# Performance work log

Hardware: AMD Instinct MI355X
Metric: run time of the kernel (lower is better)

## Reference

```python
import jax, jax.numpy as jnp
import numpy as np

_SAMPLING_EPS = 1e-5


def _apply_top_p_top_k(logits, p, k):
    # Descending sort over vocab, as in the torch.jit.script kernel.
    sort_idx = jnp.argsort(logits, axis=-1)[:, ::-1]            # [B, V]
    logits_sort = jnp.take_along_axis(logits, sort_idx, axis=-1)
    probs_sort = jax.nn.softmax(logits_sort, axis=-1)
    probs_sum = jnp.cumsum(probs_sort, axis=-1)
    ar = jnp.arange(logits.shape[-1], dtype=jnp.int32)
    mask = (probs_sum - probs_sort > p[:, None]) | (ar[None, :] >= k[:, None])
    logits_sort = jnp.where(mask, -jnp.inf, logits_sort)
    # Scatter back to original token order via inverse permutation.
    inv_idx = jnp.argsort(sort_idx, axis=-1)
    return jnp.take_along_axis(logits_sort, inv_idx, axis=-1)


def _apply_min_p(logits, min_p):
    probs = jax.nn.softmax(logits, axis=-1)
    top_probs = probs.max(axis=-1, keepdims=True)
    remove = probs < min_p[:, None] * top_probs
    return jnp.where(remove, -jnp.inf, logits)


def setup_inputs() -> dict:
    key = jax.random.key(0)
    ks = jax.random.split(key, 6)
    B, V = 128, 128000
    logits = jax.random.normal(ks[0], (B, V), dtype=jnp.float32) * 2.0
    temperatures = jax.random.uniform(ks[1], (B,), minval=0.5, maxval=1.5, dtype=jnp.float32)
    top_ps = jax.random.uniform(ks[2], (B,), minval=0.5, maxval=1.0, dtype=jnp.float32)
    top_ks = jax.random.randint(ks[3], (B,), 1, 1024, dtype=jnp.int32)
    min_ps = jax.random.uniform(ks[4], (B,), minval=0.0, maxval=0.1, dtype=jnp.float32)
    # q = Exponential(1); torch does probs * q^{-1} then argmax -> argmax(probs / q)
    exp_noise = jax.random.exponential(ks[5], (B, V), dtype=jnp.float32)
    return {"logits": logits, "temperatures": temperatures, "top_ps": top_ps,
            "top_ks": top_ks, "min_ps": min_ps, "exp_noise": exp_noise}


def reference(logits, temperatures, top_ps, top_ks, min_ps, exp_noise):
    # Greedy rows (temp < eps) are scaled by 1.0 in the original sampler.
    temps = jnp.where(temperatures < _SAMPLING_EPS, 1.0, temperatures)
    x = logits / temps[:, None]
    k = jnp.maximum(top_ks, 1)  # top_k == -1 maps to vocab_size upstream
    x = _apply_top_p_top_k(x, top_ps, k)
    x = _apply_min_p(x, min_ps)
    logprobs = jax.nn.log_softmax(x, axis=-1)
    probs = jnp.exp(logprobs)
    # exponential-trick multinomial sampling: argmax(probs * Exp(1)^{-1})
    sampled_tokens = jnp.argmax(probs / exp_noise, axis=-1)
    return sampled_tokens, probs, logprobs
```

## Files before the change

kernel.cpp:

```cpp
#include <hip/hip_runtime.h>
#include <cmath>

#define BROWS 128
#define VCOLS 128000
#define XHI 24.0f
#define BIN_INV 1.5238095f
#define CAP2 2048
#define ACAP 2048
#define LCAP 2048

__device__ __forceinline__ unsigned enc32(float x){
  unsigned b = __float_as_uint(x);
  return (b & 0x80000000u) ? ~b : (b | 0x80000000u);
}
__device__ __forceinline__ float dec32(unsigned e){
  unsigned b = (e & 0x80000000u) ? (e & 0x7FFFFFFFu) : ~e;
  return __uint_as_float(b);
}
__device__ __forceinline__ unsigned long long csel(unsigned long long a, unsigned long long b, bool keepmax){
  unsigned long long mx = a > b ? a : b;
  unsigned long long mn = a > b ? b : a;
  return keepmax ? mx : mn;
}
__device__ __forceinline__ void wagg_append(bool pred, unsigned long long key,
                                            int* cnt, unsigned long long* buf, int cap, int lane){
  unsigned long long mk = __ballot(pred);
  if (mk){
    int leader = __ffsll((long long)mk) - 1;
    int base;
    if (lane == leader) base = atomicAdd(cnt, __popcll(mk));
    base = __shfl(base, leader);
    if (pred){
      int pos = base + __popcll(mk & ((1ull << lane) - 1ull));
      if (pos < cap) buf[pos] = key;
    }
  }
}

__device__ __forceinline__ int binOf(float x){
  return (int)((XHI - x) * BIN_INV);
}

__global__ __launch_bounds__(256)
void k12_stats_collect(const float* __restrict__ logits, const float* __restrict__ temps,
                       const int* __restrict__ topks,
                       float* __restrict__ maxpart, float* __restrict__ spart,
                       unsigned* __restrict__ histpart,
                       unsigned long long* __restrict__ candbuf, int* __restrict__ ncc, int segc)
{
  const int bid = blockIdx.x;
  const int r = bid >> 3, c = bid & 7;
  const int tid = threadIdx.x, lane = tid & 63, col = tid & 31;
  __shared__ unsigned sh[2048];
  __shared__ float redm[4], reds[4];
  __shared__ unsigned long long lcand[LCAP];
  __shared__ int lcnt, sJsel;
  for (int i = tid; i < 2048; i += 256) sh[i] = 0u;
  if (tid == 0) lcnt = 0;
  __syncthreads();
  float t = temps[r]; if (t < 1e-5f) t = 1.0f;
  const float it = 1.0f / t;
  int kk = topks[r]; if (kk < 1) kk = 1;
  const float4* src = (const float4*)(logits + (size_t)r*VCOLS + c*16000);
  float mx = -INFINITY, s = 0.f;
  for (int f = tid; f < 4000; f += 256){
    float4 v = src[f];
    #pragma unroll
    for (int e = 0; e < 4; e++){
      float x = ((const float*)&v)[e] * it;
      mx = fmaxf(mx, x);
      s += __expf(x - XHI);
      int b = binOf(x);
      if (b < 64){ if (b < 0) b = 0; atomicAdd(&sh[(b<<5)+col], 1u); }
    }
  }
  #pragma unroll
  for (int o = 32; o > 0; o >>= 1){
    mx = fmaxf(mx, __shfl_down(mx, o));
    s += __shfl_down(s, o);
  }
  if (lane == 0){ redm[tid>>6] = mx; reds[tid>>6] = s; }
  __syncthreads();
  if (tid == 0){
    maxpart[bid] = fmaxf(fmaxf(redm[0], redm[1]), fmaxf(redm[2], redm[3]));
    spart[bid]   = reds[0] + reds[1] + reds[2] + reds[3];
  }
  if (tid < 64){
    unsigned cnt = 0;
    #pragma unroll
    for (int q = 0; q < 32; q++) cnt += sh[(tid<<5) + ((q + tid) & 31)];
    histpart[bid*64 + tid] = cnt;
    unsigned inc = cnt;
    #pragma unroll
    for (int o = 1; o < 64; o <<= 1){ unsigned v2 = __shfl_up(inc, o); if (lane >= o) inc += v2; }
    unsigned long long ball = __ballot(inc >= (unsigned)kk);
    if (tid == 0) sJsel = ball ? (__ffsll((long long)ball) - 1) : 63;
  }
  __syncthreads();
  const float thrJ = (float)(sJsel + 1);
  const int jbase = c*16000;
  {
    int f = tid;
    float4 v = src[f];
    while (true){
      int fn = f + 256;
      bool more = fn < 4000;
      float4 vn;
      if (more) vn = src[fn];
      #pragma unroll
      for (int e = 0; e < 4; e++){
        float x = ((const float*)&v)[e] * it;
        float vv = (XHI - x) * BIN_INV;
        bool pred = vv < thrJ;
        unsigned long long key = ((unsigned long long)enc32(x) << 32) | (unsigned)(jbase + 4*f + e);
        wagg_append(pred, key, &lcnt, lcand, LCAP, lane);
      }
      if (!more) break;
      v = vn; f = fn;
    }
  }
  __syncthreads();
  int n = lcnt; if (n > LCAP) n = LCAP; if (n > segc) n = segc;
  if (tid == 0) ncc[bid] = n;
  unsigned long long* dst = candbuf + (size_t)bid*segc;
  for (int i = tid; i < n; i += 256) dst[i] = lcand[i];
}

__global__ __launch_bounds__(1024)
void k3_select(const float* __restrict__ temps,
               const float* __restrict__ topps, const int* __restrict__ topks,
               const float* __restrict__ minps,
               const float* __restrict__ maxpart, const float* __restrict__ spart,
               const unsigned* __restrict__ histpart,
               const unsigned long long* __restrict__ candbuf, const int* __restrict__ ncc, int segc,
               const float* __restrict__ noise, float* __restrict__ out)
{
  const int r = blockIdx.x;
  const int tid = threadIdx.x;
  const int lane = tid & 63;
  __shared__ unsigned long long buf2[CAP2];
  __shared__ unsigned long long actA[ACAP];
  __shared__ unsigned long long actB[ACAP];
  __shared__ float sM, sS, sP, sMinp, sSp, swsum[16];
  __shared__ float sLogZ, sZsum;
  __shared__ int sK, sJsel, sN2, sNact, sNact2, sFbSel, sTot, sM1, sM2;
  __shared__ unsigned sFh[16];
  __shared__ unsigned long long spk[16];

  if (tid == 0){
    float M = -INFINITY; float ssum = 0.f;
    #pragma unroll
    for (int c2 = 0; c2 < 8; c2++) M = fmaxf(M, maxpart[8*r + c2]);
    #pragma unroll
    for (int c2 = 0; c2 < 8; c2++) ssum += spart[8*r + c2];
    sM = M;
    sS = expf(XHI - M) * ssum;
    int kk = topks[r]; if (kk < 1) kk = 1; sK = kk;
    sP = topps[r]; sMinp = minps[r];
    sN2 = 0; sNact = 0;
  }
  {
    int kk0 = topks[r]; if (kk0 < 1) kk0 = 1;
    if (tid < 64){
      unsigned cnt = 0;
      #pragma unroll
      for (int c2 = 0; c2 < 8; c2++) cnt += histpart[(8*r + c2)*64 + tid];
      unsigned inc = cnt;
      #pragma unroll
      for (int o = 1; o < 64; o <<= 1){ unsigned v = __shfl_up(inc, o); if (lane >= o) inc += v; }
      unsigned long long ball = __ballot(inc >= (unsigned)kk0);
      if (tid == 0) sJsel = ball ? (__ffsll((long long)ball) - 1) : 63;
    }
  }
  __syncthreads();
  const float M = sM, S = sS;
  const int kk = sK, jsel = sJsel;
  const float thrJ = (float)(jsel + 1);
  const float vLoJ = (float)jsel;
  for (int c2 = 0; c2 < 8; c2++){
    int nc = ncc[8*r + c2]; if (nc > segc) nc = segc;
    const unsigned long long* seg = candbuf + (size_t)(8*r + c2)*segc;
    int ncr = (nc + 1023) & ~1023;
    for (int i = tid; i < ncr; i += 1024){
      bool in = i < nc;
      unsigned long long key = in ? seg[i] : 0ull;
      float vv = 0.f;
      if (in){
        float x = dec32((unsigned)(key >> 32));
        vv = (XHI - x) * BIN_INV;
      }
      bool toBuf = in && (vv < vLoJ);
      bool toAct = in && !(vv < vLoJ) && (vv < thrJ);
      wagg_append(toBuf, key, &sN2, buf2, CAP2, lane);
      wagg_append(toAct, key, &sNact, actA, ACAP, lane);
    }
  }
  __syncthreads();
  int n2c  = sN2   < CAP2 ? sN2   : CAP2;
  int nact = sNact < ACAP ? sNact : ACAP;
  unsigned long long* cur = actA;
  unsigned long long* nxt = actB;
  float vLo = vLoJ, W = 1.0f;
  bool doneRoute = false;
  for (int lev = 0; lev < 4 && !doneRoute; ++lev){
    if (n2c + nact <= 1024) break;
    if (tid < 16) sFh[tid] = 0u;
    __syncthreads();
    const float inv = 16.0f / W;
    const float w16 = W * 0.0625f;
    const int nr = (nact + 1023) & ~1023;
    for (int i = tid; i < nr; i += 1024){
      if (i < nact){
        float x = dec32((unsigned)(cur[i] >> 32));
        float vv = (XHI - x) * BIN_INV;
        int fb = (int)((vv - vLo) * inv);
        fb = fb < 0 ? 0 : (fb > 15 ? 15 : fb);
        atomicAdd(&sFh[fb], 1u);
      }
    }
    __syncthreads();
    if (tid < 64){
      unsigned incv = (lane < 16) ? sFh[lane] : 0u;
      #pragma unroll
      for (int o = 1; o < 16; o <<= 1){ unsigned u = __shfl_up(incv, o); if (lane >= o) incv += u; }
      unsigned long long ball = __ballot((lane < 16) && (n2c + (int)incv >= kk));
      int fbS = ball ? (__ffsll((long long)ball) - 1) : 15;
      if (lane == fbS){ sFbSel = fbS; sTot = n2c + (int)incv; }
    }
    __syncthreads();
    const int fbSel = sFbSel;
    const int tot = sTot;
    const bool finalR = (tot <= 1024) || (lev == 3);
    if (tid == 0) sNact2 = 0;
    __syncthreads();
    for (int i = tid; i < nr; i += 1024){
      bool in = i < nact;
      unsigned long long key = in ? cur[i] : 0ull;
      int fb = 16;
      if (in){
        float x = dec32((unsigned)(key >> 32));
        float vv = (XHI - x) * BIN_INV;
        fb = (int)((vv - vLo) * inv);
        fb = fb < 0 ? 0 : (fb > 15 ? 15 : fb);
      }
      bool toBuf = in && ((fb < fbSel) || (finalR && fb == fbSel));
      bool toAct = in && !finalR && (fb == fbSel);
      wagg_append(toBuf, key, &sN2, buf2, CAP2, lane);
      wagg_append(toAct, key, &sNact2, nxt, ACAP, lane);
    }
    __syncthreads();
    n2c = sN2 < CAP2 ? sN2 : CAP2;
    if (finalR){ nact = 0; doneRoute = true; }
    else {
      nact = sNact2 < ACAP ? sNact2 : ACAP;
      unsigned long long* t2 = cur; cur = nxt; nxt = t2;
      vLo = vLo + (float)fbSel * w16;
      W = w16;
    }
  }
  if (nact > 0){
    for (int i = tid; i < nact; i += 1024){
      int pos = n2c + i; if (pos < CAP2) buf2[pos] = cur[i];
    }
    n2c = (n2c + nact < CAP2) ? (n2c + nact) : CAP2;
  }
  __syncthreads();
  const int n2 = n2c;
  const int sortN = (n2 <= 1024) ? 1024 : 2048;
  for (int i = n2 + tid; i < sortN; i += 1024) buf2[i] = 0ull;
  __syncthreads();
  if (sortN == 1024){
    unsigned long long a = buf2[tid];
    for (int ks = 2; ks <= 1024; ks <<= 1){
      for (int j = ks >> 1; j > 0; j >>= 1){
        if (j >= 64){
          __syncthreads();
          buf2[tid] = a;
          __syncthreads();
          unsigned long long b = buf2[tid ^ j];
          bool km = ((tid & ks) == 0) == ((tid & j) == 0);
          a = csel(a, b, km);
        } else {
          unsigned long long b = __shfl_xor(a, j);
          bool km = ((tid & ks) == 0) == ((lane & j) == 0);
          a = csel(a, b, km);
        }
      }
    }
    __syncthreads();
    buf2[tid] = a;
    __syncthreads();
  } else {
    unsigned long long a0 = buf2[tid], a1 = buf2[tid + 1024];
    const int i1 = tid + 1024;
    for (int ks = 2; ks <= 2048; ks <<= 1){
      for (int j = ks >> 1; j > 0; j >>= 1){
        if (j == 1024){
          unsigned long long mx = a0 > a1 ? a0 : a1;
          unsigned long long mn = a0 > a1 ? a1 : a0;
          a0 = mx; a1 = mn;
        } else if (j >= 64){
          __syncthreads();
          buf2[tid] = a0; buf2[i1] = a1;
          __syncthreads();
          unsigned long long b0 = buf2[tid ^ j];
          unsigned long long b1 = buf2[i1 ^ j];
          bool km0 = ((tid & ks) == 0) == ((tid & j) == 0);
          bool km1 = ((i1  & ks) == 0) == ((i1  & j) == 0);
          a0 = csel(a0, b0, km0);
          a1 = csel(a1, b1, km1);
        } else {
          unsigned long long b0 = __shfl_xor(a0, j);
          unsigned long long b1 = __shfl_xor(a1, j);
          bool lw = ((lane & j) == 0);
          bool km0 = (((tid & ks) == 0) == lw);
          bool km1 = (((i1  & ks) == 0) == lw);
          a0 = csel(a0, b0, km0);
          a1 = csel(a1, b1, km1);
        }
      }
    }
    __syncthreads();
    buf2[tid] = a0; buf2[i1] = a1;
    __syncthreads();
  }
  const int kk2 = kk < n2 ? kk : n2;
  if (tid == 0) sM1 = kk2;
  unsigned long long mykey = 0ull;
  float xv = 0.f, qq = 0.f;
  if (tid < kk2){
    mykey = buf2[tid];
    xv = dec32((unsigned)(mykey >> 32));
    qq = expf(xv - M);
  }
  float inc = qq;
  #pragma unroll
  for (int o = 1; o < 64; o <<= 1){ float v = __shfl_up(inc, o); if (lane >= o) inc += v; }
  if (lane == 63) swsum[tid >> 6] = inc;
  __syncthreads();
  if (tid < 16){
    float v = swsum[tid];
    #pragma unroll
    for (int o = 1; o < 16; o <<= 1){ float u = __shfl_up(v, o); if (lane >= o) v += u; }
    swsum[tid] = v;
  }
  __syncthreads();
  float epre = __shfl_up(inc, 1); if (lane == 0) epre = 0.f;
  const int wvi = tid >> 6;
  const float excl = (wvi ? swsum[wvi - 1] : 0.f) + epre;
  const float pS = sP * S;
  if (tid < kk2 && !(excl <= pS)) atomicMin(&sM1, tid);
  __syncthreads();
  const int m = sM1 > 0 ? sM1 : 1;
  if (tid == m) sSp = excl;
  if (tid == 0) sM2 = m;
  __syncthreads();
  const float Sp = sSp;
  {
    float rhs = sMinp * (1.0f / Sp);
    if (tid < m && (qq / Sp < rhs)) atomicMin(&sM2, tid);
  }
  __syncthreads();
  const int m2 = sM2 > 0 ? sM2 : 1;
  if (tid == m2) sZsum = excl;
  __syncthreads();
  if (tid == 0) sLogZ = logf(sZsum);
  __syncthreads();
  {
    const float logZ = sLogZ;
    unsigned long long pk = 0ull;
    if (tid < m2){
      unsigned idx = (unsigned)(mykey & 0xFFFFFFFFull);
      float lp = (xv - M) - logZ;
      float pr = expf(lp);
      out[128 + (size_t)r*VCOLS + idx] = pr;
      out[128 + (size_t)BROWS*VCOLS + (size_t)r*VCOLS + idx] = lp;
      float nz = noise[(size_t)r*VCOLS + idx];
      float ratio = pr / nz;
      pk = ((unsigned long long)__float_as_uint(ratio) << 32) | (unsigned)(~idx);
    }
    #pragma unroll
    for (int o = 32; o > 0; o >>= 1){
      unsigned long long other = __shfl_down(pk, o);
      if (other > pk) pk = other;
    }
    if (lane == 0) spk[tid >> 6] = pk;
    __syncthreads();
    if (tid == 0){
      unsigned long long b0 = spk[0];
      #pragma unroll
      for (int w = 1; w < 16; w++) if (spk[w] > b0) b0 = spk[w];
      out[r] = (float)(~(unsigned)(b0 & 0xFFFFFFFFull));
    }
  }
}

extern "C" void kernel_launch(void* const* d_in, const int* in_sizes, int n_in,
                              void* d_out, int out_size, void* d_ws, size_t ws_size,
                              hipStream_t stream) {
  const float* logits = (const float*)d_in[0];
  const float* temps  = (const float*)d_in[1];
  const float* topps  = (const float*)d_in[2];
  const int*   topks  = (const int*)d_in[3];
  const float* minps  = (const float*)d_in[4];
  const float* noise  = (const float*)d_in[5];
  float* out = (float*)d_out;
  char* ws = (char*)d_ws;
  float* maxpart = (float*)(ws);
  float* spart   = (float*)(ws + 4096);
  int* ncc       = (int*)(ws + 8192);
  unsigned* histpart = (unsigned*)(ws + 12288);
  unsigned long long* candbuf = (unsigned long long*)(ws + 274432);
  int segc = 2048;
  if (ws_size < (size_t)274432 + 1024ull*2048ull*8ull) segc = 1536;
  if (ws_size < (size_t)274432 + 1024ull*1536ull*8ull) segc = 512;

  k12_stats_collect<<<1024, 256, 0, stream>>>(logits, temps, topks,
                                              maxpart, spart, histpart, candbuf, ncc, segc);
  k3_select<<<128, 1024, 0, stream>>>(temps, topps, topks, minps,
                                      maxpart, spart, histpart, candbuf, ncc, segc,
                                      noise, out);
}
```

Measured before the change: 258.0 us.

## Prefetch logits loads, flatten candidate gather, merge top-p and min-p cutoffs

The first pass now double-buffers float4 loads two iterations ahead so global loads overlap the histogram and exp work. In the select kernel, segment offsets are prefix-summed once so all candidates are gathered in one flat loop instead of eight padded per-segment loops. The histogram scan moves to a second wavefront. The min-p test is rewritten as qq < minp, since the top probability maps to exp(0)=1, which lets the top-p and min-p cutoffs be found in one pass and drops two barriers. The min-p rewrite assumes the first sorted candidate is the row max and that the exp comparison matches within float rounding.

After: 257.5 us. Within noise of the previous version (-0.2%).

```diff
diff --git a/kernel.cpp b/kernel.cpp
--- a/kernel.cpp
+++ b/kernel.cpp
@@ -63,15 +63,27 @@
   int kk = topks[r]; if (kk < 1) kk = 1;
   const float4* src = (const float4*)(logits + (size_t)r*VCOLS + c*16000);
   float mx = -INFINITY, s = 0.f;
-  for (int f = tid; f < 4000; f += 256){
+  {
+    int f = tid;
     float4 v = src[f];
-    #pragma unroll
-    for (int e = 0; e < 4; e++){
-      float x = ((const float*)&v)[e] * it;
-      mx = fmaxf(mx, x);
-      s += __expf(x - XHI);
-      int b = binOf(x);
-      if (b < 64){ if (b < 0) b = 0; atomicAdd(&sh[(b<<5)+col], 1u); }
+    int f1 = f + 256;
+    bool h1 = f1 < 4000;
+    float4 v1; if (h1) v1 = src[f1];
+    while (true){
+      int f2 = f + 512;
+      bool h2 = f2 < 4000;
+      float4 v2; if (h2) v2 = src[f2];
+      #pragma unroll
+      for (int e = 0; e < 4; e++){
+        float x = ((const float*)&v)[e] * it;
+        mx = fmaxf(mx, x);
+        s += __expf(x - XHI);
+        int b = binOf(x);
+        if (b < 64){ if (b < 0) b = 0; atomicAdd(&sh[(b<<5)+col], 1u); }
+      }
+      if (!h1) break;
+      f = f1; v = v1;
+      f1 = f2; h1 = h2; v1 = v2;
     }
   }
   #pragma unroll
@@ -141,9 +153,10 @@
   __shared__ unsigned long long buf2[CAP2];
   __shared__ unsigned long long actA[ACAP];
   __shared__ unsigned long long actB[ACAP];
-  __shared__ float sM, sS, sP, sMinp, sSp, swsum[16];
+  __shared__ float sM, sS, sP, sMinp, swsum[16];
   __shared__ float sLogZ, sZsum;
   __shared__ int sK, sJsel, sN2, sNact, sNact2, sFbSel, sTot, sM1, sM2;
+  __shared__ int ssegBase[8], sTotCand;
   __shared__ unsigned sFh[16];
   __shared__ unsigned long long spk[16];
 
@@ -159,17 +172,25 @@
     sP = topps[r]; sMinp = minps[r];
     sN2 = 0; sNact = 0;
   }
+  if (tid < 64){
+    int nc = 0;
+    if (lane < 8){ nc = ncc[8*r + lane]; if (nc > segc) nc = segc; }
+    int pre = nc;
+    #pragma unroll
+    for (int o = 1; o < 8; o <<= 1){ int u = __shfl_up(pre, o); if (lane >= o) pre += u; }
+    if (lane < 8 && tid < 8){ ssegBase[lane] = pre - nc; if (lane == 7) sTotCand = pre; }
+  }
   {
     int kk0 = topks[r]; if (kk0 < 1) kk0 = 1;
-    if (tid < 64){
+    if (tid >= 64 && tid < 128){
       unsigned cnt = 0;
       #pragma unroll
-      for (int c2 = 0; c2 < 8; c2++) cnt += histpart[(8*r + c2)*64 + tid];
+      for (int c2 = 0; c2 < 8; c2++) cnt += histpart[(8*r + c2)*64 + lane];
       unsigned inc = cnt;
       #pragma unroll
       for (int o = 1; o < 64; o <<= 1){ unsigned v = __shfl_up(inc, o); if (lane >= o) inc += v; }
       unsigned long long ball = __ballot(inc >= (unsigned)kk0);
-      if (tid == 0) sJsel = ball ? (__ffsll((long long)ball) - 1) : 63;
+      if (lane == 0) sJsel = ball ? (__ffsll((long long)ball) - 1) : 63;
     }
   }
   __syncthreads();
@@ -177,15 +198,19 @@
   const int kk = sK, jsel = sJsel;
   const float thrJ = (float)(jsel + 1);
   const float vLoJ = (float)jsel;
-  for (int c2 = 0; c2 < 8; c2++){
-    int nc = ncc[8*r + c2]; if (nc > segc) nc = segc;
-    const unsigned long long* seg = candbuf + (size_t)(8*r + c2)*segc;
-    int ncr = (nc + 1023) & ~1023;
-    for (int i = tid; i < ncr; i += 1024){
-      bool in = i < nc;
-      unsigned long long key = in ? seg[i] : 0ull;
+  {
+    const int totc = sTotCand;
+    const int totr = (totc + 1023) & ~1023;
+    const unsigned long long* rowseg = candbuf + (size_t)(8*r)*segc;
+    for (int i = tid; i < totr; i += 1024){
+      bool in = i < totc;
+      unsigned long long key = 0ull;
       float vv = 0.f;
       if (in){
+        int c2 = 0;
+        #pragma unroll
+        for (int j = 1; j < 8; j++) c2 += (i >= ssegBase[j]);
+        key = rowseg[(size_t)c2*segc + (i - ssegBase[c2])];
         float x = dec32((unsigned)(key >> 32));
         vv = (XHI - x) * BIN_INV;
       }
@@ -325,7 +350,7 @@
     __syncthreads();
   }
   const int kk2 = kk < n2 ? kk : n2;
-  if (tid == 0) sM1 = kk2;
+  if (tid == 0){ sM1 = kk2; sM2 = kk2; }
   unsigned long long mykey = 0ull;
   float xv = 0.f, qq = 0.f;
   if (tid < kk2){
@@ -349,19 +374,14 @@
   const int wvi = tid >> 6;
   const float excl = (wvi ? swsum[wvi - 1] : 0.f) + epre;
   const float pS = sP * S;
-  if (tid < kk2 && !(excl <= pS)) atomicMin(&sM1, tid);
+  const float minp = sMinp;
+  if (tid < kk2){
+    if (!(excl <= pS)) atomicMin(&sM1, tid);
+    if (qq < minp)     atomicMin(&sM2, tid);
+  }
   __syncthreads();
   const int m = sM1 > 0 ? sM1 : 1;
-  if (tid == m) sSp = excl;
-  if (tid == 0) sM2 = m;
-  __syncthreads();
-  const float Sp = sSp;
-  {
-    float rhs = sMinp * (1.0f / Sp);
-    if (tid < m && (qq / Sp < rhs)) atomicMin(&sM2, tid);
-  }
-  __syncthreads();
-  const int m2 = sM2 > 0 ? sM2 : 1;
+  int m2 = sM2 < m ? sM2 : m; if (m2 < 1) m2 = 1;
   if (tid == m2) sZsum = excl;
   __syncthreads();
   if (tid == 0) sLogZ = logf(sZsum);
```
